# Performance work log

Measured on AMD Instinct MI355X. Metric: run time of the kernel, lower is better.

## Reference

```python
import jax, jax.numpy as jnp
import numpy as np

# ---- geometry / physics constants (from setup_params) ----
H = 400; W_CROP = 400
PSF_W = 121          # interpolated_psf_width
CLEAR = 20           # clear_dist
_m = int(np.ceil(PSF_W / 2 - CLEAR + 2))
MARGIN = _m + _m % 2                    # 44
IM = H + 2 * MARGIN                     # 488
MAG = 100.0; PX_CCD = 11.0              # M, pixel_size_CCD
NZ = 64; Z_MIN = -2.0; Z_MAX = 2.0      # psf bank z sampling
SIGMA_READ = 10.0                       # read noise std (counts)
N_EMIT = 2048


def setup_inputs() -> dict:
    key = jax.random.key(0)
    k1, k2, k3, k4 = jax.random.split(key, 4)
    # emitter positions (um): xy in [-15,15] (stays inside canvas), z in [-2,2]
    lo = jnp.array([-15.0, -15.0, Z_MIN], jnp.float32)
    hi = jnp.array([15.0, 15.0, Z_MAX], jnp.float32)
    local_xyz = jax.random.uniform(k1, (1, N_EMIT, 3), jnp.float32) * (hi - lo) + lo
    Nphotons = jax.random.uniform(k2, (1, N_EMIT), jnp.float32) * 4000.0 + 1000.0
    xy_center = jnp.zeros((2,), jnp.float32)  # FOV center; unused when fd_flag=False
    psf_bank = jax.random.uniform(k3, (NZ, PSF_W, PSF_W), jnp.float32)  # positive PSFs
    noise_map = jax.random.normal(k4, (H, W_CROP), jnp.float32)         # unit gaussians
    return {"local_xyz": local_xyz, "Nphotons": Nphotons, "xy_center": xy_center,
            "psf_bank": psf_bank, "noise_map": noise_map}


def reference(local_xyz, Nphotons, xy_center, psf_bank, noise_map):
    x = local_xyz[0, :, 0]                       # [N] um
    y = local_xyz[0, :, 1]
    z = local_xyz[0, :, 2]
    nph = Nphotons[0]                            # [N]

    # psf_module(0,0,z): nearest-z lookup in precomputed bank (fd_flag=False)
    zi = jnp.clip(jnp.round((z - Z_MIN) / (Z_MAX - Z_MIN) * (NZ - 1)),
                  0, NZ - 1).astype(jnp.int32)
    psf = psf_bank[zi]                           # [N, PSF_W, PSF_W]

    # emitter position in camera pixels
    lx = x * MAG / PX_CCD
    ly = y * MAG / PX_CCD
    r0f = ly + IM / 2 - PSF_W / 2
    c0f = lx + IM / 2 - PSF_W / 2
    r0 = jnp.floor(r0f).astype(jnp.int32)        # [N] integer splat origin
    c0 = jnp.floor(c0f).astype(jnp.int32)
    rs = (r0f - jnp.floor(r0f))[:, None, None]   # sub-pixel shift in [0,1)
    cs = (c0f - jnp.floor(c0f))[:, None, None]

    # sub-pixel shift (bilinear, zero-fill boundary): out[i,j] = in[i-rs, j-cs]
    P = jnp.pad(psf, ((0, 0), (1, 0), (1, 0)))
    sh = ((1 - rs) * (1 - cs) * P[:, 1:, 1:] + rs * (1 - cs) * P[:, :-1, 1:]
          + (1 - rs) * cs * P[:, 1:, :-1] + rs * cs * P[:, :-1, :-1])
    sh = jnp.abs(sh)
    sh = sh / sh.sum(axis=(1, 2), keepdims=True) * nph[:, None, None]

    # scatter-add splat into shared canvas
    ar = jnp.arange(PSF_W, dtype=jnp.int32)
    rows = r0[:, None, None] + ar[None, :, None]  # [N, PSF_W, 1]
    cols = c0[:, None, None] + ar[None, None, :]  # [N, 1, PSF_W]
    canvas = jnp.zeros((IM, IM), sh.dtype).at[rows, cols].add(sh)

    im = canvas[MARGIN:MARGIN + H, MARGIN:MARGIN + W_CROP]

    # NoiseLayer: Gaussian approx of Poisson shot + read noise
    im_noisy = im + jnp.sqrt(jnp.maximum(im, 0.0) + SIGMA_READ ** 2) * noise_map

    # project_01 normalization
    return (im_noisy - im_noisy.min()) / (im_noisy.max() - im_noisy.min())
```

## Files before the change

### kernel.cpp

```cpp
#include <hip/hip_runtime.h>

#define H        400
#define W_CROP   400
#define PSF_W    121
#define MARGIN   44
#define IM       488
#define NZ       64
#define N_EMIT   2048
#define PSF_AREA (PSF_W * PSF_W)
#define SIGMA2   100.0f
#define TILE     16
#define TB       25
#define NTILES   (TB * TB)
#define NPIX     (H * W_CROP)
#define PADW     152
#define PADA     (PADW * PADW)
#define CHUNKS   4
#define CAPC     224
#define CAP_B    512
#define NBUCK    (TB * CHUNKS)
#define PADBLK   512

typedef __fp16 h2 __attribute__((ext_vector_type(2)));

#if __has_builtin(__builtin_amdgcn_fdot2)
#define FDOT2(a, b, c) __builtin_amdgcn_fdot2((a), (b), (c), false)
#else
static __device__ __forceinline__ float FDOT2(h2 a, h2 b, float c) {
    return fmaf((float)a.x, (float)b.x, fmaf((float)a.y, (float)b.y, c));
}
#endif

static __device__ __forceinline__ unsigned pkh2(float lo, float hi) {
    const h2 v = __builtin_amdgcn_cvt_pkrtz(lo, hi);
    return __builtin_bit_cast(unsigned, v);
}

static __device__ __forceinline__ unsigned enc_ord(float f) {
    unsigned u = __float_as_uint(f);
    return (u & 0x80000000u) ? ~u : (u | 0x80000000u);
}
static __device__ __forceinline__ float dec_ord(unsigned u) {
    return __uint_as_float((u & 0x80000000u) ? (u & 0x7fffffffu) : ~u);
}

static __device__ __forceinline__ void geom_of(const float* __restrict__ xyz, int e,
                                               int& r0, int& c0, int& zi,
                                               float& r0f, float& c0f) {
    const float x = xyz[3 * e + 0];
    const float y = xyz[3 * e + 1];
    const float z = xyz[3 * e + 2];
    const float lx = (x * 100.0f) / 11.0f;
    const float ly = (y * 100.0f) / 11.0f;
    r0f = (ly + 244.0f) - 60.5f;
    c0f = (lx + 244.0f) - 60.5f;
    r0 = (int)floorf(r0f);
    c0 = (int)floorf(c0f);
    zi = (int)rintf((z + 2.0f) / 4.0f * 63.0f);
    zi = min(max(zi, 0), NZ - 1);
}

__global__ __launch_bounds__(256) void prep_kernel(
        const float* __restrict__ psf_bank, float* __restrict__ zpart,
        unsigned* __restrict__ pad, unsigned* __restrict__ minmax,
        const float* __restrict__ xyz, const float* __restrict__ nph_arr,
        float4* __restrict__ bucket, int* __restrict__ bcnt)
{
    __shared__ float red[4][4];
    __shared__ int   wtot[4];

    if (blockIdx.x < PADBLK) {
        const int zi   = blockIdx.x >> 3;
        const int part = blockIdx.x & 7;

        if (blockIdx.x == 0 && threadIdx.x == 0) { minmax[0] = 0xFFFFFFFFu; minmax[1] = 0u; }

        const float* __restrict__ src = psf_bank + (size_t)zi * PSF_AREA;
        unsigned* __restrict__ dst = pad + (size_t)zi * PADA;

        const int plo = part * 2888;
        const int phi = min(plo + 2888, PADA);
        for (int i = plo + (int)threadIdx.x; i < phi; i += 256) {
            const int rp = i / PADW;
            const int r = rp - 16;
            const int c = i - rp * PADW - 16;
            const bool rin = (unsigned)r < (unsigned)PSF_W;
            const float vm = (rin && (unsigned)(c - 1) < (unsigned)PSF_W) ? src[r * PSF_W + c - 1] : 0.0f;
            const float vc = (rin && (unsigned)c < (unsigned)PSF_W)       ? src[r * PSF_W + c]     : 0.0f;
            dst[i] = pkh2(vm, vc);
        }

        const int slo = part * 1831;
        const int shi = min(slo + 1831, PSF_AREA);
        float S = 0.f, R = 0.f, C = 0.f, K = 0.f;
        for (int i = slo + (int)threadIdx.x; i < shi; i += 256) {
            const float v = src[i];
            const int r = i / PSF_W;
            const int c = i - r * PSF_W;
            S += v;
            if (r == PSF_W - 1) R += v;
            if (c == PSF_W - 1) C += v;
            if (r == PSF_W - 1 && c == PSF_W - 1) K += v;
        }
        #pragma unroll
        for (int off = 32; off > 0; off >>= 1) {
            S += __shfl_down(S, off, 64);
            R += __shfl_down(R, off, 64);
            C += __shfl_down(C, off, 64);
            K += __shfl_down(K, off, 64);
        }
        const int wave = threadIdx.x >> 6, lane = threadIdx.x & 63;
        if (lane == 0) { red[wave][0] = S; red[wave][1] = R; red[wave][2] = C; red[wave][3] = K; }
        __syncthreads();
        if (threadIdx.x == 0) {
            float4 o;
            o.x = (red[0][0] + red[1][0]) + (red[2][0] + red[3][0]);
            o.y = (red[0][1] + red[1][1]) + (red[2][1] + red[3][1]);
            o.z = (red[0][2] + red[1][2]) + (red[2][2] + red[3][2]);
            o.w = (red[0][3] + red[1][3]) + (red[2][3] + red[3][3]);
            *(float4*)(zpart + (size_t)(zi * 8 + part) * 4) = o;
        }
        return;
    }

    const int b   = blockIdx.x - PADBLK;
    const int btr = b >> 2, bzc = b & 3;
    const int w    = threadIdx.x >> 6;
    const int lane = threadIdx.x & 63;

    int mycnt = 0;
    unsigned mymask = 0u;
    #pragma unroll
    for (int q = 0; q < 8; ++q) {
        const int e = (int)threadIdx.x * 8 + q;
        int r0, c0, zi; float r0f, c0f;
        geom_of(xyz, e, r0, c0, zi, r0f, c0f);
        const bool p = ((zi >> 4) == bzc)
                     && (btr >= ((r0 - MARGIN) >> 4)) && (btr <= ((r0 + 76) >> 4));
        mymask |= (unsigned)p << q;
        mycnt += (int)p;
    }

    int incl = mycnt;
    #pragma unroll
    for (int off = 1; off < 64; off <<= 1) {
        const int v = __shfl_up(incl, off, 64);
        if (lane >= off) incl += v;
    }
    if (lane == 63) wtot[w] = incl;
    __syncthreads();
    int base = incl - mycnt;
    #pragma unroll
    for (int ww = 0; ww < 4; ++ww) base += (ww < w) ? wtot[ww] : 0;
    const int ntot = wtot[0] + wtot[1] + wtot[2] + wtot[3];

    if (mymask) {
        int slot = base;
        #pragma unroll
        for (int q = 0; q < 8; ++q) {
            if (mymask & (1u << q)) {
                const int e = (int)threadIdx.x * 8 + q;
                int r0, c0, zi; float r0f, c0f;
                geom_of(xyz, e, r0, c0, zi, r0f, c0f);
                if (slot < CAP_B) {
                    const float rs = r0f - floorf(r0f);
                    const float cs = c0f - floorf(c0f);
                    const float nph = nph_arr[e];
                    float4 s0, s1;
                    s0.x = nph * (1.0f - rs) * (1.0f - cs);
                    s0.y = nph * (1.0f - rs) * cs;
                    s0.z = nph * rs * (1.0f - cs);
                    s0.w = nph * rs * cs;
                    const int packed = ((r0 + 16) << 15) | ((c0 + 16) << 6) | zi;
                    s1.x = rs; s1.y = cs; s1.z = __int_as_float(packed); s1.w = 0.f;
                    bucket[(size_t)(b * CAP_B + slot) * 2]     = s0;
                    bucket[(size_t)(b * CAP_B + slot) * 2 + 1] = s1;
                }
                ++slot;
            }
        }
    }
    if (threadIdx.x == 0) bcnt[b] = min(ntot, CAP_B);
}

__global__ __launch_bounds__(256) void gather_kernel(
        const unsigned* __restrict__ pad, const float4* __restrict__ bucket,
        const int* __restrict__ bcnt, const float* __restrict__ zpart,
        float* __restrict__ parts)
{
    const int zc   = (blockIdx.x & 7) >> 1;
    const int tile = 2 * (blockIdx.x >> 3) + (blockIdx.x & 1);
    if (tile >= NTILES) return;

    __shared__ float4 smeta[CAPC];
    __shared__ float  tilepart[4][256];
    __shared__ int    wtot[4];

    const int tr = tile / TB, tc = tile - tr * TB;
    const int w    = threadIdx.x >> 6;
    const int lane = threadIdx.x & 63;
    const int px = lane & 15;
    const int wy = lane >> 4;
    const int orow0 = tr * TILE + wy * 4;
    const int ocol  = tc * TILE + px;
    const int crow0 = orow0 + MARGIN;
    const int ccol  = ocol + MARGIN;
    const int tcb   = (crow0 * PADW + ccol) * 4;
    const char* __restrict__ pbase = (const char*)pad;

    const int b   = tr * CHUNKS + zc;
    const int n_b = bcnt[b];
    const float4* __restrict__ bk = bucket + (size_t)b * CAP_B * 2;

    int nstaged = 0;
    for (int base_i = 0; base_i < n_b; base_i += 256) {
        const int i = base_i + (int)threadIdx.x;
        float4 m0, m1;
        int r0 = 0, c0 = 0, zi = 0;
        bool p = false;
        if (i < n_b) {
            m0 = bk[2 * i];
            m1 = bk[2 * i + 1];
            const int packed = __float_as_int(m1.z);
            zi = packed & 63;
            c0 = ((packed >> 6) & 511) - 16;
            r0 = ((packed >> 15) & 511) - 16;
            p = (tc >= ((c0 - MARGIN) >> 4)) && (tc <= ((c0 + 76) >> 4));
        }
        int incl = (int)p;
        #pragma unroll
        for (int off = 1; off < 64; off <<= 1) {
            const int v = __shfl_up(incl, off, 64);
            if (lane >= off) incl += v;
        }
        if (lane == 63) wtot[w] = incl;
        __syncthreads();
        int slot = nstaged + incl - (int)p;
        #pragma unroll
        for (int ww = 0; ww < 4; ++ww) slot += (ww < w) ? wtot[ww] : 0;
        const int round_tot = wtot[0] + wtot[1] + wtot[2] + wtot[3];
        if (p && slot < CAPC) {
            const float rs = m1.x, cs = m1.y;
            const float4* __restrict__ zp = (const float4*)zpart + zi * 8;
            float4 zm = zp[0];
            #pragma unroll
            for (int u = 1; u < 8; ++u) {
                const float4 t = zp[u];
                zm.x += t.x; zm.y += t.y; zm.z += t.z; zm.w += t.w;
            }
            const float ssum = zm.x - rs * zm.y - cs * zm.z + rs * cs * zm.w;
            const float inv = 1.0f / ssum;
            float4 s;
            s.x = __uint_as_float(pkh2(m0.y * inv, m0.x * inv));
            s.y = __uint_as_float(pkh2(m0.w * inv, m0.z * inv));
            s.z = __int_as_float((zi * PADA + (15 - r0) * PADW + (16 - c0)) * 4);
            s.w = __int_as_float(((r0 + 16) << 16) | (c0 + 16));
            smeta[slot] = s;
        }
        nstaged += round_tot;
        __syncthreads();
    }
    const int n = min(nstaged, CAPC);

    float acc0[4] = {0.f, 0.f, 0.f, 0.f};
    float acc1[4] = {0.f, 0.f, 0.f, 0.f};
    float acc2[4] = {0.f, 0.f, 0.f, 0.f};
    float acc3[4] = {0.f, 0.f, 0.f, 0.f};

    auto body = [&](int j, float* acc) {
        const float4 s = smeta[j];
        const h2 wA = __builtin_bit_cast(h2, s.x);
        const h2 wB = __builtin_bit_cast(h2, s.y);
        const int off = __float_as_int(s.z);
        const int rc  = __float_as_int(s.w);
        const int pr0 = crow0 - ((rc >> 16) - 16);
        const int pc  = ccol  - ((rc & 0xFFFF) - 16);
        const char* __restrict__ p = pbase + (tcb + off);
        h2 f[5];
        #pragma unroll
        for (int i = 0; i < 5; ++i)
            f[i] = __builtin_bit_cast(h2, *(const unsigned*)(p + i * (PADW * 4)));
        const bool pcok = (unsigned)pc <= 120u;
        #pragma unroll
        for (int k = 0; k < 4; ++k) {
            float v = FDOT2(wA, f[k + 1], 0.0f);
            v = FDOT2(wB, f[k], v);
            const bool ok = pcok & ((unsigned)(pr0 + k) <= 120u);
            acc[k] += ok ? v : 0.f;
        }
    };

    int j = w;
    for (; j + 12 < n; j += 16) {
        body(j, acc0); body(j + 4, acc1); body(j + 8, acc2); body(j + 12, acc3);
    }
    for (; j < n; j += 4) body(j, acc0);

    #pragma unroll
    for (int k = 0; k < 4; ++k)
        tilepart[w][(wy * 4 + k) * 16 + px] = (acc0[k] + acc1[k]) + (acc2[k] + acc3[k]);
    __syncthreads();

    const int row = threadIdx.x >> 4, col = threadIdx.x & 15;
    const float s = ((tilepart[0][threadIdx.x] + tilepart[1][threadIdx.x]) +
                     (tilepart[2][threadIdx.x] + tilepart[3][threadIdx.x]));
    parts[(size_t)zc * NPIX + (tr * TILE + row) * W_CROP + (tc * TILE + col)] = s;
}

__global__ __launch_bounds__(256) void noise_minmax_kernel(
        const float* __restrict__ parts, const float* __restrict__ noise,
        float* __restrict__ out, unsigned* __restrict__ minmax)
{
    const int i = blockIdx.x * 256 + threadIdx.x;
    float vmin = 1e30f, vmax = -1e30f;
    if (i < NPIX / 4) {
        const float4 p0 = ((const float4*)parts)[i];
        const float4 p1 = ((const float4*)(parts + NPIX))[i];
        const float4 p2 = ((const float4*)(parts + 2 * NPIX))[i];
        const float4 p3 = ((const float4*)(parts + 3 * NPIX))[i];
        float4 im;
        im.x = (p0.x + p1.x) + (p2.x + p3.x);
        im.y = (p0.y + p1.y) + (p2.y + p3.y);
        im.z = (p0.z + p1.z) + (p2.z + p3.z);
        im.w = (p0.w + p1.w) + (p2.w + p3.w);
        const float4 nz = ((const float4*)noise)[i];
        im.x += sqrtf(fmaxf(im.x, 0.f) + SIGMA2) * nz.x;
        im.y += sqrtf(fmaxf(im.y, 0.f) + SIGMA2) * nz.y;
        im.z += sqrtf(fmaxf(im.z, 0.f) + SIGMA2) * nz.z;
        im.w += sqrtf(fmaxf(im.w, 0.f) + SIGMA2) * nz.w;
        ((float4*)out)[i] = im;
        vmin = fminf(fminf(im.x, im.y), fminf(im.z, im.w));
        vmax = fmaxf(fmaxf(im.x, im.y), fmaxf(im.z, im.w));
    }
    #pragma unroll
    for (int off = 32; off > 0; off >>= 1) {
        vmin = fminf(vmin, __shfl_down(vmin, off, 64));
        vmax = fmaxf(vmax, __shfl_down(vmax, off, 64));
    }
    if ((threadIdx.x & 63) == 0) {
        atomicMin(&minmax[0], enc_ord(vmin));
        atomicMax(&minmax[1], enc_ord(vmax));
    }
}

__global__ __launch_bounds__(256) void finalize_kernel(float* __restrict__ out,
                                                       const unsigned* __restrict__ minmax)
{
    const int i = blockIdx.x * 256 + threadIdx.x;
    if (i >= NPIX / 4) return;
    const float mn = dec_ord(minmax[0]);
    const float inv = 1.0f / (dec_ord(minmax[1]) - mn);
    float4 v = ((float4*)out)[i];
    v.x = (v.x - mn) * inv;
    v.y = (v.y - mn) * inv;
    v.z = (v.z - mn) * inv;
    v.w = (v.w - mn) * inv;
    ((float4*)out)[i] = v;
}

extern "C" void kernel_launch(void* const* d_in, const int* in_sizes, int n_in,
                              void* d_out, int out_size, void* d_ws, size_t ws_size,
                              hipStream_t stream) {
    const float* xyz      = (const float*)d_in[0];
    const float* nph      = (const float*)d_in[1];
    const float* psf_bank = (const float*)d_in[3];
    const float* noise    = (const float*)d_in[4];
    float* out = (float*)d_out;

    char* ws = (char*)d_ws;
    unsigned* minmax = (unsigned*)(ws + 0);
    float*    zpart  = (float*)(ws + 1024);
    unsigned* pad    = (unsigned*)(ws + 9216);
    float4*   bucket = (float4*)(ws + 5923840);
    int*      bcnt   = (int*)(ws + 7562240);
    float*    parts  = (float*)(ws + 7563264);

    prep_kernel<<<PADBLK + NBUCK, 256, 0, stream>>>(psf_bank, zpart, pad, minmax,
                                                    xyz, nph, bucket, bcnt);
    gather_kernel<<<2504, 256, 0, stream>>>(pad, bucket, bcnt, zpart, parts);
    noise_minmax_kernel<<<(NPIX / 4 + 255) / 256, 256, 0, stream>>>(parts, noise, out, minmax);
    finalize_kernel<<<(NPIX / 4 + 255) / 256, 256, 0, stream>>>(out, minmax);
}
```

Baseline: 56.03 us.

## Fuse noise/minmax and normalization via in-kernel grid barrier

Merges the noise+minmax kernel and the finalize kernel into one launch. It uses an atomic block counter as a software grid barrier, so the noisy values stay in registers and are normalized without being written and re-read from global memory. This removes one kernel launch and one full round trip of the output buffer. The cost is that correctness depends on all 157 blocks being resident at once, which should hold on a large GPU, and every block spin-waits at the barrier.

```diff
diff --git a/kernel.cpp b/kernel.cpp
--- a/kernel.cpp
+++ b/kernel.cpp
@@ -20,6 +20,7 @@
 #define CAP_B    512
 #define NBUCK    (TB * CHUNKS)
 #define PADBLK   512
+#define NMBLK    157
 
 typedef __fp16 h2 __attribute__((ext_vector_type(2)));
 
@@ -73,7 +74,9 @@
         const int zi   = blockIdx.x >> 3;
         const int part = blockIdx.x & 7;
 
-        if (blockIdx.x == 0 && threadIdx.x == 0) { minmax[0] = 0xFFFFFFFFu; minmax[1] = 0u; }
+        if (blockIdx.x == 0 && threadIdx.x == 0) {
+            minmax[0] = 0xFFFFFFFFu; minmax[1] = 0u; minmax[2] = 0u;
+        }
 
         const float* __restrict__ src = psf_bank + (size_t)zi * PSF_AREA;
         unsigned* __restrict__ dst = pad + (size_t)zi * PADA;
@@ -307,18 +310,19 @@
     parts[(size_t)zc * NPIX + (tr * TILE + row) * W_CROP + (tc * TILE + col)] = s;
 }
 
-__global__ __launch_bounds__(256) void noise_minmax_kernel(
+__global__ __launch_bounds__(256) void noise_norm_kernel(
         const float* __restrict__ parts, const float* __restrict__ noise,
         float* __restrict__ out, unsigned* __restrict__ minmax)
 {
     const int i = blockIdx.x * 256 + threadIdx.x;
+    const bool act = i < NPIX / 4;
+    float4 im = make_float4(0.f, 0.f, 0.f, 0.f);
     float vmin = 1e30f, vmax = -1e30f;
-    if (i < NPIX / 4) {
+    if (act) {
         const float4 p0 = ((const float4*)parts)[i];
         const float4 p1 = ((const float4*)(parts + NPIX))[i];
         const float4 p2 = ((const float4*)(parts + 2 * NPIX))[i];
         const float4 p3 = ((const float4*)(parts + 3 * NPIX))[i];
-        float4 im;
         im.x = (p0.x + p1.x) + (p2.x + p3.x);
         im.y = (p0.y + p1.y) + (p2.y + p3.y);
         im.z = (p0.z + p1.z) + (p2.z + p3.z);
@@ -328,7 +332,6 @@
         im.y += sqrtf(fmaxf(im.y, 0.f) + SIGMA2) * nz.y;
         im.z += sqrtf(fmaxf(im.z, 0.f) + SIGMA2) * nz.z;
         im.w += sqrtf(fmaxf(im.w, 0.f) + SIGMA2) * nz.w;
-        ((float4*)out)[i] = im;
         vmin = fminf(fminf(im.x, im.y), fminf(im.z, im.w));
         vmax = fmaxf(fmaxf(im.x, im.y), fmaxf(im.z, im.w));
     }
@@ -341,21 +344,25 @@
         atomicMin(&minmax[0], enc_ord(vmin));
         atomicMax(&minmax[1], enc_ord(vmax));
     }
-}
-
-__global__ __launch_bounds__(256) void finalize_kernel(float* __restrict__ out,
-                                                       const unsigned* __restrict__ minmax)
-{
-    const int i = blockIdx.x * 256 + threadIdx.x;
-    if (i >= NPIX / 4) return;
-    const float mn = dec_ord(minmax[0]);
-    const float inv = 1.0f / (dec_ord(minmax[1]) - mn);
-    float4 v = ((float4*)out)[i];
-    v.x = (v.x - mn) * inv;
-    v.y = (v.y - mn) * inv;
-    v.z = (v.z - mn) * inv;
-    v.w = (v.w - mn) * inv;
-    ((float4*)out)[i] = v;
+    __syncthreads();
+    if (threadIdx.x == 0) {
+        __threadfence();
+        atomicAdd(&minmax[2], 1u);
+    }
+    while (__hip_atomic_load(&minmax[2], __ATOMIC_ACQUIRE, __HIP_MEMORY_SCOPE_AGENT) < (unsigned)NMBLK)
+        __builtin_amdgcn_s_sleep(1);
+
+    const float mn  = dec_ord(__hip_atomic_load(&minmax[0], __ATOMIC_RELAXED, __HIP_MEMORY_SCOPE_AGENT));
+    const float mx  = dec_ord(__hip_atomic_load(&minmax[1], __ATOMIC_RELAXED, __HIP_MEMORY_SCOPE_AGENT));
+    const float inv = 1.0f / (mx - mn);
+    if (act) {
+        float4 v;
+        v.x = (im.x - mn) * inv;
+        v.y = (im.y - mn) * inv;
+        v.z = (im.z - mn) * inv;
+        v.w = (im.w - mn) * inv;
+        ((float4*)out)[i] = v;
+    }
 }
 
 extern "C" void kernel_launch(void* const* d_in, const int* in_sizes, int n_in,
@@ -378,6 +385,5 @@
     prep_kernel<<<PADBLK + NBUCK, 256, 0, stream>>>(psf_bank, zpart, pad, minmax,
                                                     xyz, nph, bucket, bcnt);
     gather_kernel<<<2504, 256, 0, stream>>>(pad, bucket, bcnt, zpart, parts);
-    noise_minmax_kernel<<<(NPIX / 4 + 255) / 256, 256, 0, stream>>>(parts, noise, out, minmax);
-    finalize_kernel<<<(NPIX / 4 + 255) / 256, 256, 0, stream>>>(out, minmax);
-}
+    noise_norm_kernel<<<NMBLK, 256, 0, stream>>>(parts, noise, out, minmax);
+}
```

New measurement: 79.93 us. 1.43x slower.
